# Optimization experiments

Measured on AMD Instinct MI355X. Metric: run time of the kernel, lower is better.

The kernel has to match this reference:

```python
import jax, jax.numpy as jnp
import numpy as np

B, N, K, C = 4, 8192, 16, 128
T = 3  # num_iterations


def _gather(x, idx):
    # x: (B, N, C), idx: (B, N, K) -> (B, N, K, C)
    return jax.vmap(lambda a, i: a[i])(x, idx)


def _linear(x, W, b):
    # torch nn.Linear convention: W is (out, in)
    return x @ W.T + b


def setup_inputs() -> dict:
    key = jax.random.key(0)
    ks = jax.random.split(key, 20)
    s = 0.05
    inp = {
        'xyz': jax.random.normal(ks[0], (B, N, 3), jnp.float32),
        'features': jax.random.normal(ks[1], (B, N, C), jnp.float32),
        'knn_idx': jax.random.randint(ks[2], (B, N, K), 0, N),
        # offset_pred: Linear(C,C) -> ReLU -> Linear(C,3)
        'off_W1': jax.random.normal(ks[3], (C, C), jnp.float32) * s,
        'off_b1': jnp.zeros((C,), jnp.float32),
        'off_W2': jax.random.normal(ks[4], (3, C), jnp.float32) * s,
        'off_b2': jnp.zeros((3,), jnp.float32),
        # per-iteration edge MLP: Linear(3+C, C) -> ReLU -> Linear(C, C)
        'edge_W1': jax.random.normal(ks[5], (T, C, 3 + C), jnp.float32) * s,
        'edge_b1': jnp.zeros((T, C), jnp.float32),
        'edge_W2': jax.random.normal(ks[6], (T, C, C), jnp.float32) * s,
        'edge_b2': jnp.zeros((T, C), jnp.float32),
        # per-iteration update MLP: Linear(2C, C) -> ReLU -> Linear(C, C)
        'upd_W1': jax.random.normal(ks[7], (T, C, 2 * C), jnp.float32) * s,
        'upd_b1': jnp.zeros((T, C), jnp.float32),
        'upd_W2': jax.random.normal(ks[8], (T, C, C), jnp.float32) * s,
        'upd_b2': jnp.zeros((T, C), jnp.float32),
    }
    return inp


def reference(xyz, features, knn_idx, off_W1, off_b1, off_W2, off_b2,
              edge_W1, edge_b1, edge_W2, edge_b2,
              upd_W1, upd_b1, upd_W2, upd_b2):
    n_iter = edge_W1.shape[0]
    for t in range(n_iter):
        delta_xyz = _linear(jax.nn.relu(_linear(features, off_W1, off_b1)), off_W2, off_b2)
        neighbor_xyz = _gather(xyz, knn_idx)          # (B,N,K,3)
        neighbor_feat = _gather(features, knn_idx)    # (B,N,K,C)
        center_xyz = xyz + delta_xyz                  # (B,N,3)
        rel_pos = neighbor_xyz - center_xyz[:, :, None, :]
        edge_input = jnp.concatenate([rel_pos, neighbor_feat], axis=-1)  # (B,N,K,3+C)
        edge_feat = _linear(jax.nn.relu(_linear(edge_input, edge_W1[t], edge_b1[t])), edge_W2[t], edge_b2[t])
        agg_feat = jnp.max(edge_feat, axis=2)         # (B,N,C)
        upd_in = jnp.concatenate([agg_feat, features], axis=-1)
        features = features + _linear(jax.nn.relu(_linear(upd_in, upd_W1[t], upd_b1[t])), upd_W2[t], upd_b2[t])
    return features
```

## Files before the change

kernel.cpp:

```cpp
#include <hip/hip_runtime.h>
#include <cstddef>

#define NB 4
#define NP 8192
#define NK 16
#define NC 128
#define HW_ 136
#define GIW 136
#define AGW 136
#define CW  132
#define UINW 264
#define HUW 136

using short8   = __attribute__((ext_vector_type(8))) short;
using ushort4v = __attribute__((ext_vector_type(4))) unsigned short;
using floatx4  = __attribute__((ext_vector_type(4))) float;

union U8 { short8 s8; unsigned u[4]; };

__device__ __forceinline__ unsigned short f2bf(float f) {
    union { float f; unsigned u; } v; v.f = f;
    unsigned r = v.u + 0x7FFFu + ((v.u >> 16) & 1u);
    return (unsigned short)(r >> 16);
}
__device__ __forceinline__ float bf2f(unsigned short u) {
    union { unsigned u; float f; } v; v.u = ((unsigned)u) << 16;
    return v.f;
}
__device__ __forceinline__ unsigned cvt_pk_bf16(float lo, float hi) {
    unsigned d;
    asm("v_cvt_pk_bf16_f32 %0, %1, %2" : "=v"(d) : "v"(lo), "v"(hi));
    return d;
}

#define MFMA(a, b, c) __builtin_amdgcn_mfma_f32_16x16x32_bf16((a), (b), (c), 0, 0, 0)

__device__ __forceinline__ short8 xform(short8 g, floatx4 ca, floatx4 cb) {
    U8 u;
    u.u[0] = cvt_pk_bf16(fmaxf(bf2f((unsigned short)g[0]) - ca[0], 0.f),
                         fmaxf(bf2f((unsigned short)g[1]) - ca[1], 0.f));
    u.u[1] = cvt_pk_bf16(fmaxf(bf2f((unsigned short)g[2]) - ca[2], 0.f),
                         fmaxf(bf2f((unsigned short)g[3]) - ca[3], 0.f));
    u.u[2] = cvt_pk_bf16(fmaxf(bf2f((unsigned short)g[4]) - cb[0], 0.f),
                         fmaxf(bf2f((unsigned short)g[5]) - cb[1], 0.f));
    u.u[3] = cvt_pk_bf16(fmaxf(bf2f((unsigned short)g[6]) - cb[2], 0.f),
                         fmaxf(bf2f((unsigned short)g[7]) - cb[3], 0.f));
    return u.s8;
}

__global__ void pack_weights_k(const float* __restrict__ offW1,
                               const float* __restrict__ eW1,
                               const float* __restrict__ eW2,
                               const float* __restrict__ uW1,
                               const float* __restrict__ uW2,
                               unsigned short* __restrict__ offW1p,
                               unsigned short* __restrict__ eW1fp,
                               unsigned short* __restrict__ eW2p,
                               unsigned short* __restrict__ uW1p,
                               unsigned short* __restrict__ uW2p)
{
    int i = blockIdx.x * 256 + threadIdx.x;
    if (i < 16384) { offW1p[i] = f2bf(offW1[i]); return; }
    i -= 16384;
    if (i < 49152) {
        int tt = i / 16384, rem = i % 16384;
        int o = rem / 128, k = rem % 128;
        eW1fp[i] = f2bf(eW1[(tt * 128 + o) * 131 + 3 + k]);
        return;
    }
    i -= 49152;
    if (i < 49152) { eW2p[i] = f2bf(eW2[i]); return; }
    i -= 49152;
    if (i < 98304) { uW1p[i] = f2bf(uW1[i]); return; }
    i -= 98304;
    if (i < 49152) { uW2p[i] = f2bf(uW2[i]); }
}

__global__ __launch_bounds__(256, 4)
void center_k(const float* __restrict__ Fin, const float* __restrict__ xyz,
              const unsigned short* __restrict__ offW1p,
              const float* __restrict__ offW2, const float* __restrict__ offb1,
              const float* __restrict__ offb2,
              const unsigned short* __restrict__ eW1fp,
              const float* __restrict__ eW1r0,
              const float* __restrict__ eb1_0,
              unsigned short* __restrict__ Gbf, float* __restrict__ ctr)
{
    __shared__ __align__(16) unsigned short sA[32 * HW_];
    __shared__ __align__(16) unsigned short sH[32 * HW_];
    __shared__ float s_XY[96];
    const int t = threadIdx.x, wv = t >> 6, ln = t & 63, q = ln >> 4, r = ln & 15;
    const int cg0 = wv << 1;
    const int base = blockIdx.x * 32;

    {
        int row = t >> 3, c16 = (t & 7) * 16;
        const float* src = Fin + (size_t)(base + row) * NC + c16;
        float4 f0 = *(const float4*)src;
        float4 f1 = *(const float4*)(src + 4);
        float4 f2 = *(const float4*)(src + 8);
        float4 f3 = *(const float4*)(src + 12);
        short8 u0, u1;
        u0[0]=f2bf(f0.x); u0[1]=f2bf(f0.y); u0[2]=f2bf(f0.z); u0[3]=f2bf(f0.w);
        u0[4]=f2bf(f1.x); u0[5]=f2bf(f1.y); u0[6]=f2bf(f1.z); u0[7]=f2bf(f1.w);
        u1[0]=f2bf(f2.x); u1[1]=f2bf(f2.y); u1[2]=f2bf(f2.z); u1[3]=f2bf(f2.w);
        u1[4]=f2bf(f3.x); u1[5]=f2bf(f3.y); u1[6]=f2bf(f3.z); u1[7]=f2bf(f3.w);
        *(short8*)&sA[row * HW_ + c16]     = u0;
        *(short8*)&sA[row * HW_ + c16 + 8] = u1;
    }
    if (t < 96) s_XY[t] = xyz[(size_t)base * 3 + t];
    __syncthreads();

    floatx4 agk[2][2];
    {
        short8 wo[2][4], wg[2][4];
#pragma unroll
        for (int c = 0; c < 2; ++c)
#pragma unroll
            for (int ks = 0; ks < 4; ++ks) {
                wo[c][ks] = *(const short8*)(offW1p + ((cg0 + c) * 16 + r) * NC + ks * 32 + q * 8);
                wg[c][ks] = *(const short8*)(eW1fp  + ((cg0 + c) * 16 + r) * NC + ks * 32 + q * 8);
            }
        float bo[2] = { offb1[cg0 * 16 + r], offb1[(cg0 + 1) * 16 + r] };
#pragma unroll
        for (int rt = 0; rt < 2; ++rt) {
            short8 af[4];
#pragma unroll
            for (int ks = 0; ks < 4; ++ks)
                af[ks] = *(const short8*)&sA[(rt * 16 + r) * HW_ + ks * 32 + q * 8];
            floatx4 ao[2] = { {0.f,0.f,0.f,0.f}, {0.f,0.f,0.f,0.f} };
            floatx4 ag[2] = { {0.f,0.f,0.f,0.f}, {0.f,0.f,0.f,0.f} };
#pragma unroll
            for (int c = 0; c < 2; ++c)
#pragma unroll
                for (int ks = 0; ks < 4; ++ks) {
                    ao[c] = MFMA(af[ks], wo[c][ks], ao[c]);
                    ag[c] = MFMA(af[ks], wg[c][ks], ag[c]);
                }
#pragma unroll
            for (int c = 0; c < 2; ++c) {
                int col = (cg0 + c) * 16 + r;
#pragma unroll
                for (int i = 0; i < 4; ++i)
                    sH[(rt * 16 + q * 4 + i) * HW_ + col] = f2bf(fmaxf(ao[c][i] + bo[c], 0.f));
                agk[rt][c] = ag[c];
            }
        }
    }
    __syncthreads();

    {
#pragma unroll
        for (int c = 0; c < 2; ++c) {
            int col = (cg0 + c) * 16 + r;
            const float* wN = eW1r0 + (size_t)col * 131;
            float w0 = wN[0], w1 = wN[1], w2 = wN[2], b1v = eb1_0[col];
#pragma unroll
            for (int rt = 0; rt < 2; ++rt)
#pragma unroll
                for (int i = 0; i < 4; ++i) {
                    int row = rt * 16 + q * 4 + i;
                    sA[row * HW_ + col] = f2bf(agk[rt][c][i]
                        + s_XY[row * 3 + 0] * w0 + s_XY[row * 3 + 1] * w1
                        + s_XY[row * 3 + 2] * w2 + b1v);
                }
        }
    }
    if (wv < 2) {
        int rt = wv;
        short8 wf[4];
#pragma unroll
        for (int ks = 0; ks < 4; ++ks) {
            short8 u = {0,0,0,0,0,0,0,0};
            if (r < 3) {
                const float* w = offW2 + r * NC + ks * 32 + q * 8;
                float4 f0 = *(const float4*)w;
                float4 f1 = *(const float4*)(w + 4);
                u[0]=f2bf(f0.x); u[1]=f2bf(f0.y); u[2]=f2bf(f0.z); u[3]=f2bf(f0.w);
                u[4]=f2bf(f1.x); u[5]=f2bf(f1.y); u[6]=f2bf(f1.z); u[7]=f2bf(f1.w);
            }
            wf[ks] = u;
        }
        short8 af[4];
#pragma unroll
        for (int ks = 0; ks < 4; ++ks)
            af[ks] = *(const short8*)&sH[(rt * 16 + r) * HW_ + ks * 32 + q * 8];
        floatx4 acc = {0.f, 0.f, 0.f, 0.f};
#pragma unroll
        for (int ks = 0; ks < 4; ++ks)
            acc = MFMA(af[ks], wf[ks], acc);
        if (r < 3) {
#pragma unroll
            for (int i = 0; i < 4; ++i) {
                int p = rt * 16 + q * 4 + i;
                ctr[(size_t)(base + p) * 3 + r] =
                    xyz[(size_t)(base + p) * 3 + r] + acc[i] + offb2[r];
            }
        }
    }
    __syncthreads();

    {
        int row = t >> 3, c16 = (t & 7) * 16;
        *(short8*)(Gbf + (size_t)(base + row) * NC + c16)     = *(short8*)&sA[row * HW_ + c16];
        *(short8*)(Gbf + (size_t)(base + row) * NC + c16 + 8) = *(short8*)&sA[row * HW_ + c16 + 8];
    }
}

__global__ __launch_bounds__(256, 2)
void edge_k(const unsigned short* __restrict__ Gbf,
            const int* __restrict__ knn,
            const float* __restrict__ ctr,
            const float* __restrict__ eW1rC,
            const float* __restrict__ eb2,
            const unsigned short* __restrict__ eW2p,
            unsigned short* __restrict__ aggG)
{
    __shared__ __align__(16) unsigned short s_H[64 * GIW];
    __shared__ __align__(16) float s_C[8 * CW];
    __shared__ __align__(16) unsigned short s_AGB[8 * AGW];

    const int xcd  = blockIdx.x & 7;
    const int slot = blockIdx.x >> 3;
    const int b    = xcd >> 1;
    const int n0   = ((slot << 1) | (xcd & 1)) << 3;
    const int t = threadIdx.x, wv = t >> 6, ln = t & 63;
    const int q = ln >> 4, r = ln & 15, cg0 = wv << 1;
    const int base = b * NP + n0;
    const int rr = t >> 4, c8 = (t & 15) * 8;

    const int* kb = knn + (size_t)base * NK;
    int kn[8];
#pragma unroll
    for (int j = 0; j < 8; ++j) kn[j] = kb[j * 16 + rr];
    short8 g0[4];
#pragma unroll
    for (int p = 0; p < 4; ++p)
        g0[p] = *(const short8*)(Gbf + (size_t)(b * NP + kn[p]) * NC + c8);

    short8 wf2[2][4];
#pragma unroll
    for (int c = 0; c < 2; ++c)
#pragma unroll
        for (int ks = 0; ks < 4; ++ks)
            wf2[c][ks] = *(const short8*)(eW2p + ((cg0 + c) * 16 + r) * NC + ks * 32 + q * 8);
    float eb2v[2] = { eb2[cg0 * 16 + r], eb2[(cg0 + 1) * 16 + r] };

    {
        int p = t >> 5, c0 = (t & 31) * 4;
        float cx = ctr[(size_t)(base + p) * 3 + 0];
        float cy = ctr[(size_t)(base + p) * 3 + 1];
        float cz = ctr[(size_t)(base + p) * 3 + 2];
#pragma unroll
        for (int k = 0; k < 4; ++k) {
            int col = c0 + k;
            const float* w = eW1rC + (size_t)col * 131;
            s_C[p * CW + col] = cx * w[0] + cy * w[1] + cz * w[2];
        }
    }
    __syncthreads();

#pragma unroll
    for (int p = 0; p < 4; ++p) {
        const float* cp = &s_C[p * CW + c8];
        floatx4 ca = *(const floatx4*)(cp);
        floatx4 cb = *(const floatx4*)(cp + 4);
        *(short8*)&s_H[(p * 16 + rr) * GIW + c8] = xform(g0[p], ca, cb);
    }
    short8 g1[4];
#pragma unroll
    for (int p = 0; p < 4; ++p)
        g1[p] = *(const short8*)(Gbf + (size_t)(b * NP + kn[4 + p]) * NC + c8);
    __syncthreads();

#pragma unroll
    for (int rt = 0; rt < 4; ++rt) {
        short8 af[4];
#pragma unroll
        for (int ks = 0; ks < 4; ++ks)
            af[ks] = *(const short8*)&s_H[(rt * 16 + r) * GIW + ks * 32 + q * 8];
        floatx4 acc[2] = { {0.f,0.f,0.f,0.f}, {0.f,0.f,0.f,0.f} };
#pragma unroll
        for (int c = 0; c < 2; ++c)
#pragma unroll
            for (int ks = 0; ks < 4; ++ks)
                acc[c] = MFMA(af[ks], wf2[c][ks], acc[c]);
#pragma unroll
        for (int c = 0; c < 2; ++c) {
            float m = fmaxf(fmaxf(acc[c][0], acc[c][1]), fmaxf(acc[c][2], acc[c][3]));
            m = fmaxf(m, __shfl_xor(m, 16));
            m = fmaxf(m, __shfl_xor(m, 32));
            if (q == 0)
                s_AGB[rt * AGW + (cg0 + c) * 16 + r] = f2bf(m + eb2v[c]);
        }
    }
    __syncthreads();

#pragma unroll
    for (int p = 0; p < 4; ++p) {
        const float* cp = &s_C[(4 + p) * CW + c8];
        floatx4 ca = *(const floatx4*)(cp);
        floatx4 cb = *(const floatx4*)(cp + 4);
        *(short8*)&s_H[(p * 16 + rr) * GIW + c8] = xform(g1[p], ca, cb);
    }
    __syncthreads();

#pragma unroll
    for (int rt = 0; rt < 4; ++rt) {
        short8 af[4];
#pragma unroll
        for (int ks = 0; ks < 4; ++ks)
            af[ks] = *(const short8*)&s_H[(rt * 16 + r) * GIW + ks * 32 + q * 8];
        floatx4 acc[2] = { {0.f,0.f,0.f,0.f}, {0.f,0.f,0.f,0.f} };
#pragma unroll
        for (int c = 0; c < 2; ++c)
#pragma unroll
            for (int ks = 0; ks < 4; ++ks)
                acc[c] = MFMA(af[ks], wf2[c][ks], acc[c]);
#pragma unroll
        for (int c = 0; c < 2; ++c) {
            float m = fmaxf(fmaxf(acc[c][0], acc[c][1]), fmaxf(acc[c][2], acc[c][3]));
            m = fmaxf(m, __shfl_xor(m, 16));
            m = fmaxf(m, __shfl_xor(m, 32));
            if (q == 0)
                s_AGB[(4 + rt) * AGW + (cg0 + c) * 16 + r] = f2bf(m + eb2v[c]);
        }
    }
    __syncthreads();

    if (t < 128) {
        int row = t >> 4, cc = (t & 15) * 8;
        *(short8*)(aggG + (size_t)(base + row) * NC + cc) = *(short8*)&s_AGB[row * AGW + cc];
    }
}

__global__ __launch_bounds__(256, 4)
void upd_k(const float* __restrict__ Fin, float* __restrict__ Fout,
           const unsigned short* __restrict__ aggG,
           const float* __restrict__ xyz,
           const unsigned short* __restrict__ uW1p,
           const unsigned short* __restrict__ uW2p,
           const float* __restrict__ ub1, const float* __restrict__ ub2,
           const unsigned short* __restrict__ eW1fpN,
           const float* __restrict__ eW1rN,
           const float* __restrict__ eb1N,
           const unsigned short* __restrict__ offW1p,
           const float* __restrict__ offW2, const float* __restrict__ offb1,
           const float* __restrict__ offb2,
           unsigned short* __restrict__ Gbf, float* __restrict__ ctrOut,
           int doNext)
{
    __shared__ __align__(16) unsigned short s_UIN[16 * UINW];
    __shared__ __align__(16) unsigned short s_H[16 * HUW];
    __shared__ __align__(16) unsigned short s_FN[16 * HUW];
    __shared__ float s_XY[48];

    const int t = threadIdx.x, wv = t >> 6, ln = t & 63;
    const int q = ln >> 4, r = ln & 15, cg0 = wv << 1;
    const int base = blockIdx.x * 16;
    const int row16 = t >> 4, c8 = (t & 15) * 8;

    {
        short8 av = *(const short8*)(aggG + (size_t)(base + row16) * NC + c8);
        *(short8*)&s_UIN[row16 * UINW + c8] = av;
        const float* src = Fin + (size_t)(base + row16) * NC + c8;
        float4 f0 = *(const float4*)src;
        float4 f1 = *(const float4*)(src + 4);
        short8 u;
        u[0]=f2bf(f0.x); u[1]=f2bf(f0.y); u[2]=f2bf(f0.z); u[3]=f2bf(f0.w);
        u[4]=f2bf(f1.x); u[5]=f2bf(f1.y); u[6]=f2bf(f1.z); u[7]=f2bf(f1.w);
        *(short8*)&s_UIN[row16 * UINW + 128 + c8] = u;
    }
    if (t < 48) s_XY[t] = xyz[(size_t)base * 3 + t];
    __syncthreads();

    {
        short8 wfa[2][8];
#pragma unroll
        for (int c = 0; c < 2; ++c)
#pragma unroll
            for (int ks = 0; ks < 8; ++ks)
                wfa[c][ks] = *(const short8*)(uW1p + ((cg0 + c) * 16 + r) * 256 + ks * 32 + q * 8);
        float ub1v[2] = { ub1[cg0 * 16 + r], ub1[(cg0 + 1) * 16 + r] };
        short8 af[8];
#pragma unroll
        for (int ks = 0; ks < 8; ++ks)
            af[ks] = *(const short8*)&s_UIN[r * UINW + ks * 32 + q * 8];
        floatx4 acc3[2] = { {0.f,0.f,0.f,0.f}, {0.f,0.f,0.f,0.f} };
#pragma unroll
        for (int c = 0; c < 2; ++c)
#pragma unroll
            for (int ks = 0; ks < 8; ++ks)
                acc3[c] = MFMA(af[ks], wfa[c][ks], acc3[c]);
#pragma unroll
        for (int c = 0; c < 2; ++c)
#pragma unroll
            for (int i = 0; i < 4; ++i)
                s_H[(q * 4 + i) * HUW + (cg0 + c) * 16 + r] =
                    f2bf(fmaxf(acc3[c][i] + ub1v[c], 0.f));
    }
    __syncthreads();

    {
        short8 wfb[2][4];
#pragma unroll
        for (int c = 0; c < 2; ++c)
#pragma unroll
            for (int ks = 0; ks < 4; ++ks)
                wfb[c][ks] = *(const short8*)(uW2p + ((cg0 + c) * 16 + r) * NC + ks * 32 + q * 8);
        float ub2v[2] = { ub2[cg0 * 16 + r], ub2[(cg0 + 1) * 16 + r] };
        short8 af[4];
#pragma unroll
        for (int ks = 0; ks < 4; ++ks)
            af[ks] = *(const short8*)&s_H[r * HUW + ks * 32 + q * 8];
        floatx4 acc[2] = { {0.f,0.f,0.f,0.f}, {0.f,0.f,0.f,0.f} };
#pragma unroll
        for (int c = 0; c < 2; ++c)
#pragma unroll
            for (int ks = 0; ks < 4; ++ks)
                acc[c] = MFMA(af[ks], wfb[c][ks], acc[c]);
#pragma unroll
        for (int c = 0; c < 2; ++c) {
            int col = (cg0 + c) * 16 + r;
#pragma unroll
            for (int i = 0; i < 4; ++i) {
                int p = q * 4 + i;
                float fnew = Fin[(size_t)(base + p) * NC + col] + acc[c][i] + ub2v[c];
                Fout[(size_t)(base + p) * NC + col] = fnew;
                s_FN[p * HUW + col] = f2bf(fnew);
            }
        }
    }

    if (doNext) {
        __syncthreads();
        {
            short8 wg[2][4], wo[2][4];
#pragma unroll
            for (int c = 0; c < 2; ++c)
#pragma unroll
                for (int ks = 0; ks < 4; ++ks) {
                    wg[c][ks] = *(const short8*)(eW1fpN + ((cg0 + c) * 16 + r) * NC + ks * 32 + q * 8);
                    wo[c][ks] = *(const short8*)(offW1p + ((cg0 + c) * 16 + r) * NC + ks * 32 + q * 8);
                }
            float bo[2] = { offb1[cg0 * 16 + r], offb1[(cg0 + 1) * 16 + r] };
            short8 af[4];
#pragma unroll
            for (int ks = 0; ks < 4; ++ks)
                af[ks] = *(const short8*)&s_FN[r * HUW + ks * 32 + q * 8];
            floatx4 ag[2] = { {0.f,0.f,0.f,0.f}, {0.f,0.f,0.f,0.f} };
            floatx4 ao[2] = { {0.f,0.f,0.f,0.f}, {0.f,0.f,0.f,0.f} };
#pragma unroll
            for (int c = 0; c < 2; ++c)
#pragma unroll
                for (int ks = 0; ks < 4; ++ks) {
                    ag[c] = MFMA(af[ks], wg[c][ks], ag[c]);
                    ao[c] = MFMA(af[ks], wo[c][ks], ao[c]);
                }
#pragma unroll
            for (int c = 0; c < 2; ++c) {
                int col = (cg0 + c) * 16 + r;
                const float* wN = eW1rN + (size_t)col * 131;
                float w0 = wN[0], w1 = wN[1], w2 = wN[2], b1v = eb1N[col];
#pragma unroll
                for (int i = 0; i < 4; ++i) {
                    int p = q * 4 + i;
                    s_UIN[p * UINW + col] = f2bf(ag[c][i]
                        + s_XY[p * 3 + 0] * w0 + s_XY[p * 3 + 1] * w1
                        + s_XY[p * 3 + 2] * w2 + b1v);
                    s_H[p * HUW + col]    = f2bf(fmaxf(ao[c][i] + bo[c], 0.f));
                }
            }
        }
        __syncthreads();

        *(short8*)(Gbf + (size_t)(base + row16) * NC + c8) =
            *(short8*)&s_UIN[row16 * UINW + c8];

        if (wv == 0) {
            short8 wf[4];
#pragma unroll
            for (int ks = 0; ks < 4; ++ks) {
                short8 u = {0,0,0,0,0,0,0,0};
                if (r < 3) {
                    const float* w = offW2 + r * NC + ks * 32 + q * 8;
                    float4 f0 = *(const float4*)w;
                    float4 f1 = *(const float4*)(w + 4);
                    u[0]=f2bf(f0.x); u[1]=f2bf(f0.y); u[2]=f2bf(f0.z); u[3]=f2bf(f0.w);
                    u[4]=f2bf(f1.x); u[5]=f2bf(f1.y); u[6]=f2bf(f1.z); u[7]=f2bf(f1.w);
                }
                wf[ks] = u;
            }
            short8 af[4];
#pragma unroll
            for (int ks = 0; ks < 4; ++ks)
                af[ks] = *(const short8*)&s_H[r * HUW + ks * 32 + q * 8];
            floatx4 acc = {0.f, 0.f, 0.f, 0.f};
#pragma unroll
            for (int ks = 0; ks < 4; ++ks)
                acc = MFMA(af[ks], wf[ks], acc);
            if (r < 3) {
#pragma unroll
                for (int i = 0; i < 4; ++i) {
                    int p = q * 4 + i;
                    ctrOut[(size_t)(base + p) * 3 + r] =
                        xyz[(size_t)(base + p) * 3 + r] + acc[i] + offb2[r];
                }
            }
        }
    }
}

extern "C" void kernel_launch(void* const* d_in, const int* in_sizes, int n_in,
                              void* d_out, int out_size, void* d_ws, size_t ws_size,
                              hipStream_t stream)
{
    const float* xyz   = (const float*)d_in[0];
    const float* feat  = (const float*)d_in[1];
    const int*   knn   = (const int*)d_in[2];
    const float* offW1 = (const float*)d_in[3];
    const float* offb1 = (const float*)d_in[4];
    const float* offW2 = (const float*)d_in[5];
    const float* offb2 = (const float*)d_in[6];
    const float* eW1   = (const float*)d_in[7];
    const float* eb1   = (const float*)d_in[8];
    const float* eW2   = (const float*)d_in[9];
    const float* eb2   = (const float*)d_in[10];
    const float* uW1   = (const float*)d_in[11];
    const float* ub1   = (const float*)d_in[12];
    const float* uW2   = (const float*)d_in[13];
    const float* ub2   = (const float*)d_in[14];
    float* out = (float*)d_out;

    char* ws = (char*)d_ws;
    unsigned short* Gbf    = (unsigned short*)ws;
    float*          ctrb   = (float*)(ws + 8388608);
    unsigned short* offW1p = (unsigned short*)(ws + 8781824);
    unsigned short* eW1fp  = (unsigned short*)(ws + 8814592);
    unsigned short* eW2p   = (unsigned short*)(ws + 8912896);
    unsigned short* uW1p   = (unsigned short*)(ws + 9011200);
    unsigned short* uW2p   = (unsigned short*)(ws + 9207808);
    unsigned short* aggG   = (unsigned short*)(ws + 9306112);

    pack_weights_k<<<1024, 256, 0, stream>>>(offW1, eW1, eW2, uW1, uW2,
                                             offW1p, eW1fp, eW2p, uW1p, uW2p);

    center_k<<<1024, 256, 0, stream>>>(feat, xyz, offW1p, offW2,
                                       offb1, offb2, eW1fp, eW1, eb1,
                                       Gbf, ctrb);

    for (int tt = 0; tt < 3; ++tt) {
        int ntt = (tt + 1) % 3;
        edge_k<<<4096, 256, 0, stream>>>(
            Gbf, knn, ctrb,
            eW1 + (size_t)tt * 128 * 131, eb2 + tt * 128,
            eW2p + tt * 16384, aggG);
        const float* fin = (tt == 0) ? feat : out;
        upd_k<<<2048, 256, 0, stream>>>(
            fin, out, aggG, xyz,
            uW1p + tt * 32768, uW2p + tt * 16384, ub1 + tt * 128, ub2 + tt * 128,
            eW1fp + ntt * 16384, eW1 + (size_t)ntt * 128 * 131, eb1 + ntt * 128,
            offW1p, offW2, offb1, offb2,
            Gbf, ctrb, (tt < 2) ? 1 : 0);
    }
}
```

Baseline: 322.8 us.

## Process 32 points per block in upd_k and remap blocks per XCD

The update kernel now handles 32 points per block in two 16-row MFMA tiles, so each wave reuses the weight fragments it loaded from global memory across twice as many rows. The grid is halved. Block indices are remapped so that each XCD (blockIdx & 7) works on a contiguous region of one batch, which aims to improve L2 locality. This costs more LDS and registers per block and lowers launch_bounds occupancy from 4 to 3, and the smaller grid leaves less parallelism.

```diff
diff --git a/kernel.cpp b/kernel.cpp
--- a/kernel.cpp
+++ b/kernel.cpp
@@ -334,7 +334,7 @@
     }
 }
 
-__global__ __launch_bounds__(256, 4)
+__global__ __launch_bounds__(256, 3)
 void upd_k(const float* __restrict__ Fin, float* __restrict__ Fout,
            const unsigned short* __restrict__ aggG,
            const float* __restrict__ xyz,
@@ -350,28 +350,38 @@
            unsigned short* __restrict__ Gbf, float* __restrict__ ctrOut,
            int doNext)
 {
-    __shared__ __align__(16) unsigned short s_UIN[16 * UINW];
-    __shared__ __align__(16) unsigned short s_H[16 * HUW];
-    __shared__ __align__(16) unsigned short s_FN[16 * HUW];
-    __shared__ float s_XY[48];
-
+    __shared__ __align__(16) unsigned short s_UIN[32 * UINW];
+    __shared__ __align__(16) unsigned short s_H[32 * HUW];
+    __shared__ __align__(16) unsigned short s_FN[32 * HUW];
+    __shared__ float s_XY[96];
+
+    const int xcd  = blockIdx.x & 7;
+    const int slot = blockIdx.x >> 3;
+    const int b    = xcd >> 1;
+    const int n0   = ((slot << 1) | (xcd & 1)) << 5;
     const int t = threadIdx.x, wv = t >> 6, ln = t & 63;
     const int q = ln >> 4, r = ln & 15, cg0 = wv << 1;
-    const int base = blockIdx.x * 16;
-    const int row16 = t >> 4, c8 = (t & 15) * 8;
-
-    {
-        short8 av = *(const short8*)(aggG + (size_t)(base + row16) * NC + c8);
-        *(short8*)&s_UIN[row16 * UINW + c8] = av;
-        const float* src = Fin + (size_t)(base + row16) * NC + c8;
+    const int base = b * NP + n0;
+    const int row32 = t >> 3, c16 = (t & 7) * 16;
+
+    {
+        const unsigned short* ap = aggG + (size_t)(base + row32) * NC + c16;
+        *(short8*)&s_UIN[row32 * UINW + c16]     = *(const short8*)ap;
+        *(short8*)&s_UIN[row32 * UINW + c16 + 8] = *(const short8*)(ap + 8);
+        const float* src = Fin + (size_t)(base + row32) * NC + c16;
         float4 f0 = *(const float4*)src;
         float4 f1 = *(const float4*)(src + 4);
-        short8 u;
-        u[0]=f2bf(f0.x); u[1]=f2bf(f0.y); u[2]=f2bf(f0.z); u[3]=f2bf(f0.w);
-        u[4]=f2bf(f1.x); u[5]=f2bf(f1.y); u[6]=f2bf(f1.z); u[7]=f2bf(f1.w);
-        *(short8*)&s_UIN[row16 * UINW + 128 + c8] = u;
-    }
-    if (t < 48) s_XY[t] = xyz[(size_t)base * 3 + t];
+        float4 f2 = *(const float4*)(src + 8);
+        float4 f3 = *(const float4*)(src + 12);
+        short8 u0, u1;
+        u0[0]=f2bf(f0.x); u0[1]=f2bf(f0.y); u0[2]=f2bf(f0.z); u0[3]=f2bf(f0.w);
+        u0[4]=f2bf(f1.x); u0[5]=f2bf(f1.y); u0[6]=f2bf(f1.z); u0[7]=f2bf(f1.w);
+        u1[0]=f2bf(f2.x); u1[1]=f2bf(f2.y); u1[2]=f2bf(f2.z); u1[3]=f2bf(f2.w);
+        u1[4]=f2bf(f3.x); u1[5]=f2bf(f3.y); u1[6]=f2bf(f3.z); u1[7]=f2bf(f3.w);
+        *(short8*)&s_UIN[row32 * UINW + 128 + c16]     = u0;
+        *(short8*)&s_UIN[row32 * UINW + 128 + c16 + 8] = u1;
+    }
+    if (t < 96) s_XY[t] = xyz[(size_t)base * 3 + t];
     __syncthreads();
 
     {
@@ -382,22 +392,25 @@
             for (int ks = 0; ks < 8; ++ks)
                 wfa[c][ks] = *(const short8*)(uW1p + ((cg0 + c) * 16 + r) * 256 + ks * 32 + q * 8);
         float ub1v[2] = { ub1[cg0 * 16 + r], ub1[(cg0 + 1) * 16 + r] };
-        short8 af[8];
-#pragma unroll
-        for (int ks = 0; ks < 8; ++ks)
-            af[ks] = *(const short8*)&s_UIN[r * UINW + ks * 32 + q * 8];
-        floatx4 acc3[2] = { {0.f,0.f,0.f,0.f}, {0.f,0.f,0.f,0.f} };
-#pragma unroll
-        for (int c = 0; c < 2; ++c)
+#pragma unroll
+        for (int rt = 0; rt < 2; ++rt) {
+            short8 af[8];
 #pragma unroll
             for (int ks = 0; ks < 8; ++ks)
-                acc3[c] = MFMA(af[ks], wfa[c][ks], acc3[c]);
-#pragma unroll
-        for (int c = 0; c < 2; ++c)
-#pragma unroll
-            for (int i = 0; i < 4; ++i)
-                s_H[(q * 4 + i) * HUW + (cg0 + c) * 16 + r] =
-                    f2bf(fmaxf(acc3[c][i] + ub1v[c], 0.f));
+                af[ks] = *(const short8*)&s_UIN[(rt * 16 + r) * UINW + ks * 32 + q * 8];
+            floatx4 acc3[2] = { {0.f,0.f,0.f,0.f}, {0.f,0.f,0.f,0.f} };
+#pragma unroll
+            for (int c = 0; c < 2; ++c)
+#pragma unroll
+                for (int ks = 0; ks < 8; ++ks)
+                    acc3[c] = MFMA(af[ks], wfa[c][ks], acc3[c]);
+#pragma unroll
+            for (int c = 0; c < 2; ++c)
+#pragma unroll
+                for (int i = 0; i < 4; ++i)
+                    s_H[(rt * 16 + q * 4 + i) * HUW + (cg0 + c) * 16 + r] =
+                        f2bf(fmaxf(acc3[c][i] + ub1v[c], 0.f));
+        }
     }
     __syncthreads();
 
@@ -409,25 +422,28 @@
             for (int ks = 0; ks < 4; ++ks)
                 wfb[c][ks] = *(const short8*)(uW2p + ((cg0 + c) * 16 + r) * NC + ks * 32 + q * 8);
         float ub2v[2] = { ub2[cg0 * 16 + r], ub2[(cg0 + 1) * 16 + r] };
-        short8 af[4];
-#pragma unroll
-        for (int ks = 0; ks < 4; ++ks)
-            af[ks] = *(const short8*)&s_H[r * HUW + ks * 32 + q * 8];
-        floatx4 acc[2] = { {0.f,0.f,0.f,0.f}, {0.f,0.f,0.f,0.f} };
-#pragma unroll
-        for (int c = 0; c < 2; ++c)
-#pragma unroll
-            for (int ks = 0; ks < 4; ++ks)
-                acc[c] = MFMA(af[ks], wfb[c][ks], acc[c]);
-#pragma unroll
-        for (int c = 0; c < 2; ++c) {
-            int col = (cg0 + c) * 16 + r;
-#pragma unroll
-            for (int i = 0; i < 4; ++i) {
-                int p = q * 4 + i;
-                float fnew = Fin[(size_t)(base + p) * NC + col] + acc[c][i] + ub2v[c];
-                Fout[(size_t)(base + p) * NC + col] = fnew;
-                s_FN[p * HUW + col] = f2bf(fnew);
+#pragma unroll
+        for (int rt = 0; rt < 2; ++rt) {
+            short8 af[4];
+#pragma unroll
+            for (int ks = 0; ks < 4; ++ks)
+                af[ks] = *(const short8*)&s_H[(rt * 16 + r) * HUW + ks * 32 + q * 8];
+            floatx4 acc[2] = { {0.f,0.f,0.f,0.f}, {0.f,0.f,0.f,0.f} };
+#pragma unroll
+            for (int c = 0; c < 2; ++c)
+#pragma unroll
+                for (int ks = 0; ks < 4; ++ks)
+                    acc[c] = MFMA(af[ks], wfb[c][ks], acc[c]);
+#pragma unroll
+            for (int c = 0; c < 2; ++c) {
+                int col = (cg0 + c) * 16 + r;
+#pragma unroll
+                for (int i = 0; i < 4; ++i) {
+                    int p = rt * 16 + q * 4 + i;
+                    float fnew = Fin[(size_t)(base + p) * NC + col] + acc[c][i] + ub2v[c];
+                    Fout[(size_t)(base + p) * NC + col] = fnew;
+                    s_FN[p * HUW + col] = f2bf(fnew);
+                }
             }
         }
     }
@@ -444,40 +460,46 @@
                     wo[c][ks] = *(const short8*)(offW1p + ((cg0 + c) * 16 + r) * NC + ks * 32 + q * 8);
                 }
             float bo[2] = { offb1[cg0 * 16 + r], offb1[(cg0 + 1) * 16 + r] };
-            short8 af[4];
-#pragma unroll
-            for (int ks = 0; ks < 4; ++ks)
-                af[ks] = *(const short8*)&s_FN[r * HUW + ks * 32 + q * 8];
-            floatx4 ag[2] = { {0.f,0.f,0.f,0.f}, {0.f,0.f,0.f,0.f} };
-            floatx4 ao[2] = { {0.f,0.f,0.f,0.f}, {0.f,0.f,0.f,0.f} };
-#pragma unroll
-            for (int c = 0; c < 2; ++c)
-#pragma unroll
-                for (int ks = 0; ks < 4; ++ks) {
-                    ag[c] = MFMA(af[ks], wg[c][ks], ag[c]);
-                    ao[c] = MFMA(af[ks], wo[c][ks], ao[c]);
-                }
-#pragma unroll
-            for (int c = 0; c < 2; ++c) {
-                int col = (cg0 + c) * 16 + r;
-                const float* wN = eW1rN + (size_t)col * 131;
-                float w0 = wN[0], w1 = wN[1], w2 = wN[2], b1v = eb1N[col];
-#pragma unroll
-                for (int i = 0; i < 4; ++i) {
-                    int p = q * 4 + i;
-                    s_UIN[p * UINW + col] = f2bf(ag[c][i]
-                        + s_XY[p * 3 + 0] * w0 + s_XY[p * 3 + 1] * w1
-                        + s_XY[p * 3 + 2] * w2 + b1v);
-                    s_H[p * HUW + col]    = f2bf(fmaxf(ao[c][i] + bo[c], 0.f));
+#pragma unroll
+            for (int rt = 0; rt < 2; ++rt) {
+                short8 af[4];
+#pragma unroll
+                for (int ks = 0; ks < 4; ++ks)
+                    af[ks] = *(const short8*)&s_FN[(rt * 16 + r) * HUW + ks * 32 + q * 8];
+                floatx4 ag[2] = { {0.f,0.f,0.f,0.f}, {0.f,0.f,0.f,0.f} };
+                floatx4 ao[2] = { {0.f,0.f,0.f,0.f}, {0.f,0.f,0.f,0.f} };
+#pragma unroll
+                for (int c = 0; c < 2; ++c)
+#pragma unroll
+                    for (int ks = 0; ks < 4; ++ks) {
+                        ag[c] = MFMA(af[ks], wg[c][ks], ag[c]);
+                        ao[c] = MFMA(af[ks], wo[c][ks], ao[c]);
+                    }
+#pragma unroll
+                for (int c = 0; c < 2; ++c) {
+                    int col = (cg0 + c) * 16 + r;
+                    const float* wN = eW1rN + (size_t)col * 131;
+                    float w0 = wN[0], w1 = wN[1], w2 = wN[2], b1v = eb1N[col];
+#pragma unroll
+                    for (int i = 0; i < 4; ++i) {
+                        int p = rt * 16 + q * 4 + i;
+                        s_UIN[p * UINW + col] = f2bf(ag[c][i]
+                            + s_XY[p * 3 + 0] * w0 + s_XY[p * 3 + 1] * w1
+                            + s_XY[p * 3 + 2] * w2 + b1v);
+                        s_H[p * HUW + col]    = f2bf(fmaxf(ao[c][i] + bo[c], 0.f));
+                    }
                 }
             }
         }
         __syncthreads();
 
-        *(short8*)(Gbf + (size_t)(base + row16) * NC + c8) =
-            *(short8*)&s_UIN[row16 * UINW + c8];
-
-        if (wv == 0) {
+        *(short8*)(Gbf + (size_t)(base + row32) * NC + c16) =
+            *(short8*)&s_UIN[row32 * UINW + c16];
+        *(short8*)(Gbf + (size_t)(base + row32) * NC + c16 + 8) =
+            *(short8*)&s_UIN[row32 * UINW + c16 + 8];
+
+        if (wv < 2) {
+            int rt = wv;
             short8 wf[4];
 #pragma unroll
             for (int ks = 0; ks < 4; ++ks) {
@@ -494,7 +516,7 @@
             short8 af[4];
 #pragma unroll
             for (int ks = 0; ks < 4; ++ks)
-                af[ks] = *(const short8*)&s_H[r * HUW + ks * 32 + q * 8];
+                af[ks] = *(const short8*)&s_H[(rt * 16 + r) * HUW + ks * 32 + q * 8];
             floatx4 acc = {0.f, 0.f, 0.f, 0.f};
 #pragma unroll
             for (int ks = 0; ks < 4; ++ks)
@@ -502,7 +524,7 @@
             if (r < 3) {
 #pragma unroll
                 for (int i = 0; i < 4; ++i) {
-                    int p = q * 4 + i;
+                    int p = rt * 16 + q * 4 + i;
                     ctrOut[(size_t)(base + p) * 3 + r] =
                         xyz[(size_t)(base + p) * 3 + r] + acc[i] + offb2[r];
                 }
@@ -556,7 +578,7 @@
             eW1 + (size_t)tt * 128 * 131, eb2 + tt * 128,
             eW2p + tt * 16384, aggG);
         const float* fin = (tt == 0) ? feat : out;
-        upd_k<<<2048, 256, 0, stream>>>(
+        upd_k<<<1024, 256, 0, stream>>>(
             fin, out, aggG, xyz,
             uW1p + tt * 32768, uW2p + tt * 16384, ub1 + tt * 128, ub2 + tt * 128,
             eW1fp + ntt * 16384, eW1 + (size_t)ntt * 128 * 131, eb1 + ntt * 128,
```

Measured after the change: 295.9 us. -8.3%, faster.

## Fuse edge and update kernels into one per-iteration kernel with ping-pong buffers

Applied to the files above, without the earlier changes.

Merges the edge-conv kernel and the update/next-center kernel into one kernel per iteration, so the aggregated max features stay in shared memory instead of going through a global aggG buffer. The gather source and center buffers are now double-buffered, so blocks writing the next iteration's data cannot race with other blocks still gathering from the current one. The cost is that each update MFMA tile now works on only 8 valid rows padded to 16, which wastes half the MFMA work. The fused kernel also uses more shared memory per block at two blocks per CU, which may lower occupancy for the update phase.

```diff
diff --git a/kernel.cpp b/kernel.cpp
--- a/kernel.cpp
+++ b/kernel.cpp
@@ -9,8 +9,7 @@
 #define GIW 136
 #define AGW 136
 #define CW  132
-#define UINW 264
-#define HUW 136
+#define FSW 136
 
 using short8   = __attribute__((ext_vector_type(8))) short;
 using ushort4v = __attribute__((ext_vector_type(4))) unsigned short;
@@ -208,17 +207,31 @@
 }
 
 __global__ __launch_bounds__(256, 2)
-void edge_k(const unsigned short* __restrict__ Gbf,
-            const int* __restrict__ knn,
-            const float* __restrict__ ctr,
+void iter_k(const float* __restrict__ Fin, float* __restrict__ Fout,
+            const unsigned short* __restrict__ Gin,
+            const float* __restrict__ xyz, const int* __restrict__ knn,
+            const float* __restrict__ ctrIn,
             const float* __restrict__ eW1rC,
             const float* __restrict__ eb2,
             const unsigned short* __restrict__ eW2p,
-            unsigned short* __restrict__ aggG)
+            const unsigned short* __restrict__ uW1p,
+            const unsigned short* __restrict__ uW2p,
+            const float* __restrict__ ub1, const float* __restrict__ ub2,
+            const unsigned short* __restrict__ eW1fpN,
+            const float* __restrict__ eW1rN,
+            const float* __restrict__ eb1N,
+            const unsigned short* __restrict__ offW1p,
+            const float* __restrict__ offW2, const float* __restrict__ offb1,
+            const float* __restrict__ offb2,
+            unsigned short* __restrict__ Gout, float* __restrict__ ctrOut,
+            int doNext)
 {
     __shared__ __align__(16) unsigned short s_H[64 * GIW];
     __shared__ __align__(16) float s_C[8 * CW];
-    __shared__ __align__(16) unsigned short s_AGB[8 * AGW];
+    __shared__ __align__(16) unsigned short s_AGB[16 * AGW];
+    __shared__ __align__(16) unsigned short s_FSB[8 * FSW];
+    __shared__ __align__(16) unsigned short s_FN[8 * FSW];
+    __shared__ float s_XY[24];
 
     const int xcd  = blockIdx.x & 7;
     const int slot = blockIdx.x >> 3;
@@ -236,7 +249,7 @@
     short8 g0[4];
 #pragma unroll
     for (int p = 0; p < 4; ++p)
-        g0[p] = *(const short8*)(Gbf + (size_t)(b * NP + kn[p]) * NC + c8);
+        g0[p] = *(const short8*)(Gin + (size_t)(b * NP + kn[p]) * NC + c8);
 
     short8 wf2[2][4];
 #pragma unroll
@@ -248,9 +261,9 @@
 
     {
         int p = t >> 5, c0 = (t & 31) * 4;
-        float cx = ctr[(size_t)(base + p) * 3 + 0];
-        float cy = ctr[(size_t)(base + p) * 3 + 1];
-        float cz = ctr[(size_t)(base + p) * 3 + 2];
+        float cx = ctrIn[(size_t)(base + p) * 3 + 0];
+        float cy = ctrIn[(size_t)(base + p) * 3 + 1];
+        float cz = ctrIn[(size_t)(base + p) * 3 + 2];
 #pragma unroll
         for (int k = 0; k < 4; ++k) {
             int col = c0 + k;
@@ -258,6 +271,17 @@
             s_C[p * CW + col] = cx * w[0] + cy * w[1] + cz * w[2];
         }
     }
+    {
+        int row = t >> 5, c4 = (t & 31) * 4;
+        float4 f = *(const float4*)(Fin + (size_t)(base + row) * NC + c4);
+        ushort4v u = { f2bf(f.x), f2bf(f.y), f2bf(f.z), f2bf(f.w) };
+        *(ushort4v*)&s_FSB[row * FSW + c4] = u;
+    }
+    if (t < 128) {
+        short8 z = {0,0,0,0,0,0,0,0};
+        *(short8*)&s_AGB[(8 + (t >> 4)) * AGW + (t & 15) * 8] = z;
+    }
+    if (t < 24) s_XY[t] = xyz[(size_t)base * 3 + t];
     __syncthreads();
 
 #pragma unroll
@@ -270,7 +294,7 @@
     short8 g1[4];
 #pragma unroll
     for (int p = 0; p < 4; ++p)
-        g1[p] = *(const short8*)(Gbf + (size_t)(b * NP + kn[4 + p]) * NC + c8);
+        g1[p] = *(const short8*)(Gin + (size_t)(b * NP + kn[4 + p]) * NC + c8);
     __syncthreads();
 
 #pragma unroll
@@ -328,52 +352,6 @@
     }
     __syncthreads();
 
-    if (t < 128) {
-        int row = t >> 4, cc = (t & 15) * 8;
-        *(short8*)(aggG + (size_t)(base + row) * NC + cc) = *(short8*)&s_AGB[row * AGW + cc];
-    }
-}
-
-__global__ __launch_bounds__(256, 4)
-void upd_k(const float* __restrict__ Fin, float* __restrict__ Fout,
-           const unsigned short* __restrict__ aggG,
-           const float* __restrict__ xyz,
-           const unsigned short* __restrict__ uW1p,
-           const unsigned short* __restrict__ uW2p,
-           const float* __restrict__ ub1, const float* __restrict__ ub2,
-           const unsigned short* __restrict__ eW1fpN,
-           const float* __restrict__ eW1rN,
-           const float* __restrict__ eb1N,
-           const unsigned short* __restrict__ offW1p,
-           const float* __restrict__ offW2, const float* __restrict__ offb1,
-           const float* __restrict__ offb2,
-           unsigned short* __restrict__ Gbf, float* __restrict__ ctrOut,
-           int doNext)
-{
-    __shared__ __align__(16) unsigned short s_UIN[16 * UINW];
-    __shared__ __align__(16) unsigned short s_H[16 * HUW];
-    __shared__ __align__(16) unsigned short s_FN[16 * HUW];
-    __shared__ float s_XY[48];
-
-    const int t = threadIdx.x, wv = t >> 6, ln = t & 63;
-    const int q = ln >> 4, r = ln & 15, cg0 = wv << 1;
-    const int base = blockIdx.x * 16;
-    const int row16 = t >> 4, c8 = (t & 15) * 8;
-
-    {
-        short8 av = *(const short8*)(aggG + (size_t)(base + row16) * NC + c8);
-        *(short8*)&s_UIN[row16 * UINW + c8] = av;
-        const float* src = Fin + (size_t)(base + row16) * NC + c8;
-        float4 f0 = *(const float4*)src;
-        float4 f1 = *(const float4*)(src + 4);
-        short8 u;
-        u[0]=f2bf(f0.x); u[1]=f2bf(f0.y); u[2]=f2bf(f0.z); u[3]=f2bf(f0.w);
-        u[4]=f2bf(f1.x); u[5]=f2bf(f1.y); u[6]=f2bf(f1.z); u[7]=f2bf(f1.w);
-        *(short8*)&s_UIN[row16 * UINW + 128 + c8] = u;
-    }
-    if (t < 48) s_XY[t] = xyz[(size_t)base * 3 + t];
-    __syncthreads();
-
     {
         short8 wfa[2][8];
 #pragma unroll
@@ -384,8 +362,11 @@
         float ub1v[2] = { ub1[cg0 * 16 + r], ub1[(cg0 + 1) * 16 + r] };
         short8 af[8];
 #pragma unroll
-        for (int ks = 0; ks < 8; ++ks)
-            af[ks] = *(const short8*)&s_UIN[r * UINW + ks * 32 + q * 8];
+        for (int ks = 0; ks < 4; ++ks)
+            af[ks] = *(const short8*)&s_AGB[r * AGW + ks * 32 + q * 8];
+#pragma unroll
+        for (int ks = 0; ks < 4; ++ks)
+            af[4 + ks] = *(const short8*)&s_FSB[(r & 7) * FSW + ks * 32 + q * 8];
         floatx4 acc3[2] = { {0.f,0.f,0.f,0.f}, {0.f,0.f,0.f,0.f} };
 #pragma unroll
         for (int c = 0; c < 2; ++c)
@@ -396,7 +377,7 @@
         for (int c = 0; c < 2; ++c)
 #pragma unroll
             for (int i = 0; i < 4; ++i)
-                s_H[(q * 4 + i) * HUW + (cg0 + c) * 16 + r] =
+                s_H[(q * 4 + i) * GIW + (cg0 + c) * 16 + r] =
                     f2bf(fmaxf(acc3[c][i] + ub1v[c], 0.f));
     }
     __syncthreads();
@@ -412,22 +393,24 @@
         short8 af[4];
 #pragma unroll
         for (int ks = 0; ks < 4; ++ks)
-            af[ks] = *(const short8*)&s_H[r * HUW + ks * 32 + q * 8];
+            af[ks] = *(const short8*)&s_H[r * GIW + ks * 32 + q * 8];
         floatx4 acc[2] = { {0.f,0.f,0.f,0.f}, {0.f,0.f,0.f,0.f} };
 #pragma unroll
         for (int c = 0; c < 2; ++c)
 #pragma unroll
             for (int ks = 0; ks < 4; ++ks)
                 acc[c] = MFMA(af[ks], wfb[c][ks], acc[c]);
-#pragma unroll
-        for (int c = 0; c < 2; ++c) {
-            int col = (cg0 + c) * 16 + r;
-#pragma unroll
-            for (int i = 0; i < 4; ++i) {
-                int p = q * 4 + i;
-                float fnew = Fin[(size_t)(base + p) * NC + col] + acc[c][i] + ub2v[c];
-                Fout[(size_t)(base + p) * NC + col] = fnew;
-                s_FN[p * HUW + col] = f2bf(fnew);
+        if (q < 2) {
+#pragma unroll
+            for (int c = 0; c < 2; ++c) {
+                int col = (cg0 + c) * 16 + r;
+#pragma unroll
+                for (int i = 0; i < 4; ++i) {
+                    int p = q * 4 + i;
+                    float fnew = Fin[(size_t)(base + p) * NC + col] + acc[c][i] + ub2v[c];
+                    Fout[(size_t)(base + p) * NC + col] = fnew;
+                    s_FN[p * FSW + col] = f2bf(fnew);
+                }
             }
         }
     }
@@ -447,7 +430,7 @@
             short8 af[4];
 #pragma unroll
             for (int ks = 0; ks < 4; ++ks)
-                af[ks] = *(const short8*)&s_FN[r * HUW + ks * 32 + q * 8];
+                af[ks] = *(const short8*)&s_FN[(r & 7) * FSW + ks * 32 + q * 8];
             floatx4 ag[2] = { {0.f,0.f,0.f,0.f}, {0.f,0.f,0.f,0.f} };
             floatx4 ao[2] = { {0.f,0.f,0.f,0.f}, {0.f,0.f,0.f,0.f} };
 #pragma unroll
@@ -457,26 +440,30 @@
                     ag[c] = MFMA(af[ks], wg[c][ks], ag[c]);
                     ao[c] = MFMA(af[ks], wo[c][ks], ao[c]);
                 }
-#pragma unroll
-            for (int c = 0; c < 2; ++c) {
-                int col = (cg0 + c) * 16 + r;
-                const float* wN = eW1rN + (size_t)col * 131;
-                float w0 = wN[0], w1 = wN[1], w2 = wN[2], b1v = eb1N[col];
-#pragma unroll
-                for (int i = 0; i < 4; ++i) {
-                    int p = q * 4 + i;
-                    s_UIN[p * UINW + col] = f2bf(ag[c][i]
-                        + s_XY[p * 3 + 0] * w0 + s_XY[p * 3 + 1] * w1
-                        + s_XY[p * 3 + 2] * w2 + b1v);
-                    s_H[p * HUW + col]    = f2bf(fmaxf(ao[c][i] + bo[c], 0.f));
+            if (q < 2) {
+#pragma unroll
+                for (int c = 0; c < 2; ++c) {
+                    int col = (cg0 + c) * 16 + r;
+                    const float* wN = eW1rN + (size_t)col * 131;
+                    float w0 = wN[0], w1 = wN[1], w2 = wN[2], b1v = eb1N[col];
+#pragma unroll
+                    for (int i = 0; i < 4; ++i) {
+                        int p = q * 4 + i;
+                        s_H[p * GIW + col] = f2bf(ag[c][i]
+                            + s_XY[p * 3 + 0] * w0 + s_XY[p * 3 + 1] * w1
+                            + s_XY[p * 3 + 2] * w2 + b1v);
+                        s_FSB[p * FSW + col] = f2bf(fmaxf(ao[c][i] + bo[c], 0.f));
+                    }
                 }
             }
         }
         __syncthreads();
 
-        *(short8*)(Gbf + (size_t)(base + row16) * NC + c8) =
-            *(short8*)&s_UIN[row16 * UINW + c8];
-
+        if (t < 128) {
+            int row = t >> 4, cc = (t & 15) * 8;
+            *(short8*)(Gout + (size_t)(base + row) * NC + cc) =
+                *(short8*)&s_H[row * GIW + cc];
+        }
         if (wv == 0) {
             short8 wf[4];
 #pragma unroll
@@ -494,17 +481,17 @@
             short8 af[4];
 #pragma unroll
             for (int ks = 0; ks < 4; ++ks)
-                af[ks] = *(const short8*)&s_H[r * HUW + ks * 32 + q * 8];
+                af[ks] = *(const short8*)&s_FSB[(r & 7) * FSW + ks * 32 + q * 8];
             floatx4 acc = {0.f, 0.f, 0.f, 0.f};
 #pragma unroll
             for (int ks = 0; ks < 4; ++ks)
                 acc = MFMA(af[ks], wf[ks], acc);
-            if (r < 3) {
+            if (r < 3 && q < 2) {
 #pragma unroll
                 for (int i = 0; i < 4; ++i) {
                     int p = q * 4 + i;
                     ctrOut[(size_t)(base + p) * 3 + r] =
-                        xyz[(size_t)(base + p) * 3 + r] + acc[i] + offb2[r];
+                        s_XY[p * 3 + r] + acc[i] + offb2[r];
                 }
             }
         }
@@ -533,34 +520,37 @@
     float* out = (float*)d_out;
 
     char* ws = (char*)d_ws;
-    unsigned short* Gbf    = (unsigned short*)ws;
-    float*          ctrb   = (float*)(ws + 8388608);
-    unsigned short* offW1p = (unsigned short*)(ws + 8781824);
-    unsigned short* eW1fp  = (unsigned short*)(ws + 8814592);
-    unsigned short* eW2p   = (unsigned short*)(ws + 8912896);
-    unsigned short* uW1p   = (unsigned short*)(ws + 9011200);
-    unsigned short* uW2p   = (unsigned short*)(ws + 9207808);
-    unsigned short* aggG   = (unsigned short*)(ws + 9306112);
+    unsigned short* GbfA   = (unsigned short*)ws;
+    unsigned short* GbfB   = (unsigned short*)(ws + 8388608);
+    float*          ctrA   = (float*)(ws + 16777216);
+    float*          ctrB   = (float*)(ws + 17170432);
+    unsigned short* offW1p = (unsigned short*)(ws + 17563648);
+    unsigned short* eW1fp  = (unsigned short*)(ws + 17596416);
+    unsigned short* eW2p   = (unsigned short*)(ws + 17694720);
+    unsigned short* uW1p   = (unsigned short*)(ws + 17793024);
+    unsigned short* uW2p   = (unsigned short*)(ws + 17989632);
 
     pack_weights_k<<<1024, 256, 0, stream>>>(offW1, eW1, eW2, uW1, uW2,
                                              offW1p, eW1fp, eW2p, uW1p, uW2p);
 
     center_k<<<1024, 256, 0, stream>>>(feat, xyz, offW1p, offW2,
                                        offb1, offb2, eW1fp, eW1, eb1,
-                                       Gbf, ctrb);
-
+                                       GbfA, ctrA);
+
+    unsigned short* Gin = GbfA; unsigned short* Gout = GbfB;
+    float* Cin = ctrA; float* Cout = ctrB;
     for (int tt = 0; tt < 3; ++tt) {
         int ntt = (tt + 1) % 3;
-        edge_k<<<4096, 256, 0, stream>>>(
-            Gbf, knn, ctrb,
+        const float* fin = (tt == 0) ? feat : out;
+        iter_k<<<4096, 256, 0, stream>>>(
+            fin, out, Gin, xyz, knn, Cin,
             eW1 + (size_t)tt * 128 * 131, eb2 + tt * 128,
-            eW2p + tt * 16384, aggG);
-        const float* fin = (tt == 0) ? feat : out;
-        upd_k<<<2048, 256, 0, stream>>>(
-            fin, out, aggG, xyz,
+            eW2p + tt * 16384,
             uW1p + tt * 32768, uW2p + tt * 16384, ub1 + tt * 128, ub2 + tt * 128,
             eW1fp + ntt * 16384, eW1 + (size_t)ntt * 128 * 131, eb1 + ntt * 128,
             offW1p, offW2, offb1, offb2,
-            Gbf, ctrb, (tt < 2) ? 1 : 0);
-    }
-}
+            Gout, Cout, (tt < 2) ? 1 : 0);
+        unsigned short* gt = Gin; Gin = Gout; Gout = gt;
+        float* ct = Cin; Cin = Cout; Cout = ct;
+    }
+}
```

Result: slower. 405.8 us (+25.7%).
